# Kernel optimization log

Hardware: AMD Instinct MI355X
Metric: run time of the kernel (lower is better)

The kernel has to match this reference:

```python
import jax, jax.numpy as jnp
import numpy as np

T, B, E, H = 2048, 2, 1024, 16
HD = E // H  # 64


def _apply_rope(x, sin_pos, cos_pos):
    # x: [B*H, T, HD]; rotate-half interleaved variant
    rot = jnp.stack([-x[..., 1::2], x[..., ::2]], axis=-1).reshape(x.shape)
    return x * cos_pos + rot * sin_pos


def setup_inputs() -> dict:
    key = jax.random.key(0)
    ks = jax.random.split(key, 6)
    scale_in = (6.0 / (3 * E + E)) ** 0.5  # xavier_uniform bound
    scale_out = (6.0 / (E + E)) ** 0.5
    return {
        "query": jax.random.normal(ks[0], (T, B, E), dtype=jnp.float32),
        "rel_pos": jax.random.normal(ks[1], (1, T, HD), dtype=jnp.float32),
        "in_proj_weight": jax.random.uniform(ks[2], (3 * E, E), jnp.float32, -scale_in, scale_in),
        "in_proj_bias": jnp.zeros((3 * E,), jnp.float32),
        "out_proj_weight": jax.random.uniform(ks[3], (E, E), jnp.float32, -scale_out, scale_out),
        "out_proj_bias": jnp.zeros((E,), jnp.float32),
    }


def reference(query, rel_pos, in_proj_weight, in_proj_bias, out_proj_weight, out_proj_bias):
    tgt_len, bsz, embed_dim = query.shape
    scaling = HD ** -0.5
    # fused QKV projection: F.linear(query, W, b) with W [3E, E]
    qkv = jnp.einsum("tbe,fe->tbf", query, in_proj_weight) + in_proj_bias
    q, k, v = jnp.split(qkv, 3, axis=-1)
    q = q * scaling
    # [T, B, E] -> [B*H, T, HD]
    def split_heads(x):
        return jnp.transpose(x.reshape(tgt_len, bsz * H, HD), (1, 0, 2))
    q, k, v = split_heads(q), split_heads(k), split_heads(v)
    # rotary embedding: sin, cos = rel_pos.chunk(2, -1), duplicated interleaved
    sin, cos = rel_pos[..., : HD // 2], rel_pos[..., HD // 2 :]
    sin_pos = jnp.stack([sin, sin], axis=-1).reshape(rel_pos.shape)
    cos_pos = jnp.stack([cos, cos], axis=-1).reshape(rel_pos.shape)
    q = _apply_rope(q, sin_pos, cos_pos)
    k = _apply_rope(k, sin_pos, cos_pos)
    # attention
    attn_weights = jnp.einsum("bqd,bkd->bqk", q, k)  # [B*H, T, T]
    attn_weights = jax.nn.softmax(attn_weights, axis=-1)
    attn = jnp.einsum("bqk,bkd->bqd", attn_weights, v)
    # [B*H, T, HD] -> [T, B, E]
    attn = jnp.transpose(attn, (1, 0, 2)).reshape(tgt_len, bsz, embed_dim)
    out = jnp.einsum("tbe,fe->tbf", attn, out_proj_weight) + out_proj_bias
    return out
```

## Files before the change

kernel.cpp:

```cpp
#include <hip/hip_runtime.h>

#define T_  2048
#define B_  2
#define E_  1024
#define H_  16
#define HD_ 64
#define M_  4096
#define N_QKV 3072

typedef unsigned short u16;
typedef unsigned int   u32;
typedef __attribute__((ext_vector_type(8))) __bf16 bf16x8;
typedef __attribute__((ext_vector_type(4))) float  f32x4;

__device__ inline u16 f2bf(float f) {
  u32 u = __float_as_uint(f);
  u += 0x7fffu + ((u >> 16) & 1u);
  return (u16)(u >> 16);
}

__device__ inline u32 cvtpk(float lo, float hi) {
  u32 r;
  asm("v_cvt_pk_bf16_f32 %0, %1, %2" : "=v"(r) : "v"(lo), "v"(hi));
  return r;
}

__device__ inline void gl_lds16(const u16* g, u16* l) {
  __builtin_amdgcn_global_load_lds(
      (const __attribute__((address_space(1))) u32*)g,
      (__attribute__((address_space(3))) u32*)l, 16, 0, 0);
}

__device__ inline int xcd_swz(int orig, int nwg) {
  return (orig & 7) * (nwg >> 3) + (orig >> 3);
}

__global__ __launch_bounds__(256) void cvt_kernel(
    const float* __restrict__ q, const float* __restrict__ wi,
    const float* __restrict__ wo, u16* __restrict__ X,
    u16* __restrict__ Wi, u16* __restrict__ Wo) {
  int idx = blockIdx.x * 256 + threadIdx.x;
  const int n1 = (M_ * E_) / 4, n2 = (3 * E_ * E_) / 4;
  const float4* src; u16* dst; int i;
  if (idx < n1)            { src = (const float4*)q;  dst = X;  i = idx; }
  else if (idx < n1 + n2)  { src = (const float4*)wi; dst = Wi; i = idx - n1; }
  else                     { src = (const float4*)wo; dst = Wo; i = idx - n1 - n2; }
  float4 v = src[i];
  uint2 o;
  o.x = (u32)f2bf(v.x) | ((u32)f2bf(v.y) << 16);
  o.y = (u32)f2bf(v.z) | ((u32)f2bf(v.w) << 16);
  *(uint2*)&dst[(size_t)i * 4] = o;
}

__global__ __launch_bounds__(256) void gemm_qkv(
    const u16* __restrict__ X, const u16* __restrict__ W,
    const float* __restrict__ bias, const float* __restrict__ rel,
    u16* __restrict__ qb, u16* __restrict__ kp, u16* __restrict__ vp) {
  const int K = E_;
  __shared__ u16 SH[16384];
  u16 (*As)[4096] = (u16(*)[4096])SH;
  u16 (*Bs)[4096] = (u16(*)[4096])(SH + 8192);
  int orig = blockIdx.y * gridDim.x + blockIdx.x;
  int wgid = xcd_swz(orig, 32 * 24);
  const int tm = (wgid & 31) * 128, tn = (wgid >> 5) * 128;
  const int tid = threadIdx.x;
  const int w = tid >> 6, lane = tid & 63, lr = lane & 15, lg = lane >> 4;
  const int wm = (w >> 1) * 64, wn = (w & 1) * 64;
  auto stage = [&](int buf, int k0) {
    #pragma unroll
    for (int hh = 0; hh < 2; ++hh) {
      int ca = (w * 2 + hh) * 64 + lane;
      int ga = ca ^ ((ca >> 3) & 3);
      gl_lds16(X + (size_t)(tm + (ga >> 2)) * K + k0 + (ga & 3) * 8,
               &As[buf][(w * 2 + hh) * 512]);
      gl_lds16(W + (size_t)(tn + (ga >> 2)) * K + k0 + (ga & 3) * 8,
               &Bs[buf][(w * 2 + hh) * 512]);
    }
  };
  f32x4 acc[4][4] = {};
  stage(0, 0);
  __syncthreads();
  for (int it = 0; it < 32; ++it) {
    int cur = it & 1;
    if (it < 31) stage(cur ^ 1, (it + 1) * 32);
    bf16x8 af[4], bq[4];
    #pragma unroll
    for (int mi = 0; mi < 4; ++mi) {
      int ga = (wm + mi * 16 + lr) * 4 + lg; ga ^= (ga >> 3) & 3;
      af[mi] = *(const bf16x8*)&As[cur][ga * 8];
    }
    #pragma unroll
    for (int ni = 0; ni < 4; ++ni) {
      int ga = (wn + ni * 16 + lr) * 4 + lg; ga ^= (ga >> 3) & 3;
      bq[ni] = *(const bf16x8*)&Bs[cur][ga * 8];
    }
    #pragma unroll
    for (int mi = 0; mi < 4; ++mi)
      #pragma unroll
      for (int ni = 0; ni < 4; ++ni)
        acc[mi][ni] = __builtin_amdgcn_mfma_f32_16x16x32_bf16(
            af[mi], bq[ni], acc[mi][ni], 0, 0, 0);
    __syncthreads();
  }
  const int sect = tn >> 10;
  #pragma unroll
  for (int ni = 0; ni < 4; ++ni) {
    int n = tn + wn + ni * 16 + lr;
    float bv = bias[n];
    int nn = n & 1023;
    int d = nn & 63, i2 = d >> 1;
    int hsub = (nn >> 6) & 1;
    #pragma unroll
    for (int mi = 0; mi < 4; ++mi) {
      #pragma unroll
      for (int r = 0; r < 4; ++r) {
        int m = tm + wm + mi * 16 + lg * 4 + r;
        int t = m >> 1, bb = m & 1, tl = t & 63;
        float v = acc[mi][ni][r] + bv;
        if (sect == 0) v *= 0.125f;
        if (sect < 2) {
          float partner = __shfl_xor(v, 1);
          float sp = rel[t * HD_ + i2];
          float cp = rel[t * HD_ + 32 + i2];
          float rot = (d & 1) ? partner : -partner;
          v = v * cp + rot * sp;
        }
        int off;
        if (sect == 0)
          off = tl * 64 + d;
        else if (sect == 1)
          off = (((tl >> 4) * 2 + (d >> 5)) << 9)
              + (((d >> 3) & 3) << 7) + ((tl & 15) << 3) + (d & 7);
        else
          off = (((tl >> 5) * 4 + (d >> 4)) << 9)
              + (((tl >> 3) & 3) << 7) + ((d & 15) << 3) + (tl & 7);
        SH[((bb << 1) | hsub) * 4096 + off] = f2bf(v);
      }
    }
  }
  __syncthreads();
  {
    int h0 = (tn & 1023) >> 6;
    int bb = w >> 1, hs = w & 1;
    int bh = bb * H_ + h0 + hs;
    int t0 = tm >> 1;
    u16* dst;
    if (sect == 0)      dst = qb + ((size_t)bh * T_ + t0) * HD_;
    else if (sect == 1) dst = kp + (((size_t)bh * 32 + (t0 >> 6)) << 12);
    else                dst = vp + (((size_t)bh * 32 + (t0 >> 6)) << 12);
    const u16* srcp = SH + w * 4096;
    #pragma unroll
    for (int i = 0; i < 8; ++i)
      *(uint4*)&dst[(size_t)(i * 64 + lane) * 8] =
          *(const uint4*)&srcp[(i * 64 + lane) * 8];
  }
}

__global__ __launch_bounds__(256, 4) void attn_kernel(
    const u16* __restrict__ qbm, const u16* __restrict__ kp,
    const u16* __restrict__ vp, u16* __restrict__ attnb) {
  __shared__ u16 Kl[2][4096];
  __shared__ u16 Vl[2][4096];
  int orig = blockIdx.y * gridDim.x + blockIdx.x;
  int wgid = xcd_swz(orig, 32 * 32);
  int bh = wgid >> 5;
  int tid = threadIdx.x;
  int w = tid >> 6, lane = tid & 63, lr = lane & 15, lg = lane >> 4;
  int qbase = (wgid & 31) * 64 + w * 16;
  const u16* qrow  = qbm + (size_t)bh * T_ * HD_;
  const u16* ktile = kp + ((size_t)bh * 32) * 4096;
  const u16* vtile = vp + ((size_t)bh * 32) * 4096;
  bf16x8 qf[2];
  #pragma unroll
  for (int ks = 0; ks < 2; ++ks)
    qf[ks] = *(const bf16x8*)&qrow[(size_t)(qbase + lr) * HD_ + ks * 32 + lg * 8];
  const int cb0 = w * 128, cb1 = w * 128 + 64;
  gl_lds16(ktile + (size_t)(cb0 + lane) * 8, &Kl[0][cb0 * 8]);
  gl_lds16(ktile + (size_t)(cb1 + lane) * 8, &Kl[0][cb1 * 8]);
  gl_lds16(vtile + (size_t)(cb0 + lane) * 8, &Vl[0][cb0 * 8]);
  gl_lds16(vtile + (size_t)(cb1 + lane) * 8, &Vl[0][cb1 * 8]);
  f32x4 o[4] = {};
  float mrun = -INFINITY, lrun = 0.f;
  __syncthreads();
  for (int kt = 0; kt < 32; ++kt) {
    int cur = kt & 1;
    if (kt < 31) {
      const u16* kn = ktile + ((size_t)(kt + 1)) * 4096;
      const u16* vn = vtile + ((size_t)(kt + 1)) * 4096;
      gl_lds16(kn + (size_t)(cb0 + lane) * 8, &Kl[cur ^ 1][cb0 * 8]);
      gl_lds16(kn + (size_t)(cb1 + lane) * 8, &Kl[cur ^ 1][cb1 * 8]);
      gl_lds16(vn + (size_t)(cb0 + lane) * 8, &Vl[cur ^ 1][cb0 * 8]);
      gl_lds16(vn + (size_t)(cb1 + lane) * 8, &Vl[cur ^ 1][cb1 * 8]);
    }
    f32x4 st[4];
    #pragma unroll
    for (int kb4 = 0; kb4 < 4; ++kb4) {
      st[kb4] = (f32x4){0.f, 0.f, 0.f, 0.f};
      #pragma unroll
      for (int ks = 0; ks < 2; ++ks) {
        bf16x8 a = *(const bf16x8*)&Kl[cur][(kb4 * 2 + ks) * 512 + lane * 8];
        st[kb4] = __builtin_amdgcn_mfma_f32_16x16x32_bf16(a, qf[ks], st[kb4], 0, 0, 0);
      }
    }
    float mx = -INFINITY;
    #pragma unroll
    for (int kb4 = 0; kb4 < 4; ++kb4)
      #pragma unroll
      for (int r = 0; r < 4; ++r) mx = fmaxf(mx, st[kb4][r]);
    mx = fmaxf(mx, __shfl_xor(mx, 16));
    mx = fmaxf(mx, __shfl_xor(mx, 32));
    if (!__all(mx <= mrun + 8.f)) {
      float mnew = fmaxf(mrun, mx);
      float sc = __expf(mrun - mnew);
      lrun *= sc;
      #pragma unroll
      for (int db = 0; db < 4; ++db) o[db] *= sc;
      mrun = mnew;
    }
    float ls = 0.f;
    u32 cv[4][2];
    #pragma unroll
    for (int kb4 = 0; kb4 < 4; ++kb4) {
      float p0 = __expf(st[kb4][0] - mrun);
      float p1 = __expf(st[kb4][1] - mrun);
      float p2 = __expf(st[kb4][2] - mrun);
      float p3 = __expf(st[kb4][3] - mrun);
      ls += (p0 + p1) + (p2 + p3);
      cv[kb4][0] = cvtpk(p0, p1);
      cv[kb4][1] = cvtpk(p2, p3);
    }
    ls += __shfl_xor(ls, 16);
    ls += __shfl_xor(ls, 32);
    lrun += ls;
    #pragma unroll
    for (int ks = 0; ks < 2; ++ks) {
      u32 a = cv[ks * 2][0], b = cv[ks * 2][1];
      u32 c = cv[ks * 2 + 1][0], d = cv[ks * 2 + 1][1];
      asm("v_permlane32_swap_b32 %0, %1" : "+v"(a), "+v"(c));
      asm("v_permlane32_swap_b32 %0, %1" : "+v"(b), "+v"(d));
      asm("v_permlane16_swap_b32 %0, %1" : "+v"(a), "+v"(c));
      asm("v_permlane16_swap_b32 %0, %1" : "+v"(b), "+v"(d));
      u32 pf32[4] = {a, b, c, d};
      bf16x8 pf = *(const bf16x8*)pf32;
      #pragma unroll
      for (int db = 0; db < 4; ++db) {
        bf16x8 vf = *(const bf16x8*)&Vl[cur][(ks * 4 + db) * 512 + lane * 8];
        o[db] = __builtin_amdgcn_mfma_f32_16x16x32_bf16(vf, pf, o[db], 0, 0, 0);
      }
    }
    __syncthreads();
  }
  float inv = 1.f / lrun;
  int bb = bh >> 4, h = bh & 15;
  int m = (qbase + lr) * 2 + bb;
  #pragma unroll
  for (int db = 0; db < 4; ++db) {
    uint2 u;
    u.x = cvtpk(o[db][0] * inv, o[db][1] * inv);
    u.y = cvtpk(o[db][2] * inv, o[db][3] * inv);
    *(uint2*)&attnb[(size_t)m * E_ + h * 64 + db * 16 + lg * 4] = u;
  }
}

__global__ __launch_bounds__(256) void gemm_out(
    const u16* __restrict__ A, const u16* __restrict__ W,
    const float* __restrict__ bias, float* __restrict__ out) {
  const int K = E_;
  __shared__ u16 As[2][4096];
  __shared__ u16 Bs[2][4096];
  int orig = blockIdx.y * gridDim.x + blockIdx.x;
  int wgid = xcd_swz(orig, 32 * 8);
  const int tm = (wgid & 31) * 128, tn = (wgid >> 5) * 128;
  const int tid = threadIdx.x;
  const int w = tid >> 6, lane = tid & 63, lr = lane & 15, lg = lane >> 4;
  const int wm = (w >> 1) * 64, wn = (w & 1) * 64;
  auto stage = [&](int buf, int k0) {
    #pragma unroll
    for (int hh = 0; hh < 2; ++hh) {
      int ca = (w * 2 + hh) * 64 + lane;
      int ga = ca ^ ((ca >> 3) & 3);
      gl_lds16(A + (size_t)(tm + (ga >> 2)) * K + k0 + (ga & 3) * 8,
               &As[buf][(w * 2 + hh) * 512]);
      gl_lds16(W + (size_t)(tn + (ga >> 2)) * K + k0 + (ga & 3) * 8,
               &Bs[buf][(w * 2 + hh) * 512]);
    }
  };
  f32x4 acc[4][4] = {};
  stage(0, 0);
  __syncthreads();
  for (int it = 0; it < 32; ++it) {
    int cur = it & 1;
    if (it < 31) stage(cur ^ 1, (it + 1) * 32);
    bf16x8 af[4], bq[4];
    #pragma unroll
    for (int mi = 0; mi < 4; ++mi) {
      int ga = (wm + mi * 16 + lr) * 4 + lg; ga ^= (ga >> 3) & 3;
      af[mi] = *(const bf16x8*)&As[cur][ga * 8];
    }
    #pragma unroll
    for (int ni = 0; ni < 4; ++ni) {
      int ga = (wn + ni * 16 + lr) * 4 + lg; ga ^= (ga >> 3) & 3;
      bq[ni] = *(const bf16x8*)&Bs[cur][ga * 8];
    }
    #pragma unroll
    for (int mi = 0; mi < 4; ++mi)
      #pragma unroll
      for (int ni = 0; ni < 4; ++ni)
        acc[mi][ni] = __builtin_amdgcn_mfma_f32_16x16x32_bf16(
            af[mi], bq[ni], acc[mi][ni], 0, 0, 0);
    __syncthreads();
  }
  #pragma unroll
  for (int ni = 0; ni < 4; ++ni) {
    int n = tn + wn + ni * 16 + lr;
    float bv = bias[n];
    #pragma unroll
    for (int mi = 0; mi < 4; ++mi) {
      #pragma unroll
      for (int r = 0; r < 4; ++r) {
        int m = tm + wm + mi * 16 + lg * 4 + r;
        out[(size_t)m * E_ + n] = acc[mi][ni][r] + bv;
      }
    }
  }
}

extern "C" void kernel_launch(void* const* d_in, const int* in_sizes, int n_in,
                              void* d_out, int out_size, void* d_ws, size_t ws_size,
                              hipStream_t stream) {
  const float* q   = (const float*)d_in[0];
  const float* rel = (const float*)d_in[1];
  const float* wi  = (const float*)d_in[2];
  const float* bi  = (const float*)d_in[3];
  const float* wo  = (const float*)d_in[4];
  const float* bo  = (const float*)d_in[5];
  float* out = (float*)d_out;
  char* ws = (char*)d_ws;
  u16* Xb  = (u16*)(ws);
  u16* Wib = (u16*)(ws + 8388608);
  u16* Wob = (u16*)(ws + 14680064);
  u16* qb  = (u16*)(ws + 16777216);
  u16* kpb = (u16*)(ws + 25165824);
  u16* vpb = (u16*)(ws + 33554432);
  u16* attnb = Xb;

  cvt_kernel<<<dim3(8192), dim3(256), 0, stream>>>(q, wi, wo, Xb, Wib, Wob);
  gemm_qkv<<<dim3(32, 24), dim3(256), 0, stream>>>(Xb, Wib, bi, rel, qb, kpb, vpb);
  attn_kernel<<<dim3(32, 32), dim3(256), 0, stream>>>(qb, kpb, vpb, attnb);
  gemm_out<<<dim3(32, 8), dim3(256), 0, stream>>>(attnb, Wob, bo, out);
}
```

Before: 139.6 us.

## Use partial vmcnt waits with raw barriers and base-2 softmax exponent

Replaces __syncthreads in the GEMM and attention loops with explicit s_waitcnt vmcnt(4) plus raw s_barrier, so the next tile's global-to-LDS loads can stay in flight while the current tile is consumed. It also folds log2(e) into the Q scaling (0.125*1.4427) so softmax can use exp2f instead of __expf, and raises the rescale threshold to match the base-2 domain. The risk is correctness: with the wait placed after the prefetch issue, vmcnt(4) only guarantees the older loads landed, and the hand-written counts and compiler fences must match the actual number of outstanding loads per thread.

Result: slower. 153.4 us (+9.9%).

```diff
diff --git a/kernel.cpp b/kernel.cpp
--- a/kernel.cpp
+++ b/kernel.cpp
@@ -34,6 +34,9 @@
 __device__ inline int xcd_swz(int orig, int nwg) {
   return (orig & 7) * (nwg >> 3) + (orig >> 3);
 }
+
+#define BAR()   __builtin_amdgcn_s_barrier()
+#define FENCE() asm volatile("" ::: "memory")
 
 __global__ __launch_bounds__(256) void cvt_kernel(
     const float* __restrict__ q, const float* __restrict__ wi,
@@ -79,10 +82,16 @@
   };
   f32x4 acc[4][4] = {};
   stage(0, 0);
-  __syncthreads();
   for (int it = 0; it < 32; ++it) {
     int cur = it & 1;
-    if (it < 31) stage(cur ^ 1, (it + 1) * 32);
+    if (it < 31) {
+      stage(cur ^ 1, (it + 1) * 32);
+      asm volatile("s_waitcnt vmcnt(4)" ::: "memory");
+    } else {
+      asm volatile("s_waitcnt vmcnt(0)" ::: "memory");
+    }
+    BAR();
+    FENCE();
     bf16x8 af[4], bq[4];
     #pragma unroll
     for (int mi = 0; mi < 4; ++mi) {
@@ -100,7 +109,8 @@
       for (int ni = 0; ni < 4; ++ni)
         acc[mi][ni] = __builtin_amdgcn_mfma_f32_16x16x32_bf16(
             af[mi], bq[ni], acc[mi][ni], 0, 0, 0);
-    __syncthreads();
+    FENCE();
+    BAR();
   }
   const int sect = tn >> 10;
   #pragma unroll
@@ -117,7 +127,7 @@
         int m = tm + wm + mi * 16 + lg * 4 + r;
         int t = m >> 1, bb = m & 1, tl = t & 63;
         float v = acc[mi][ni][r] + bv;
-        if (sect == 0) v *= 0.125f;
+        if (sect == 0) v *= 0.18033688f;
         if (sect < 2) {
           float partner = __shfl_xor(v, 1);
           float sp = rel[t * HD_ + i2];
@@ -175,23 +185,27 @@
   for (int ks = 0; ks < 2; ++ks)
     qf[ks] = *(const bf16x8*)&qrow[(size_t)(qbase + lr) * HD_ + ks * 32 + lg * 8];
   const int cb0 = w * 128, cb1 = w * 128 + 64;
-  gl_lds16(ktile + (size_t)(cb0 + lane) * 8, &Kl[0][cb0 * 8]);
-  gl_lds16(ktile + (size_t)(cb1 + lane) * 8, &Kl[0][cb1 * 8]);
-  gl_lds16(vtile + (size_t)(cb0 + lane) * 8, &Vl[0][cb0 * 8]);
-  gl_lds16(vtile + (size_t)(cb1 + lane) * 8, &Vl[0][cb1 * 8]);
+  auto stage = [&](int buf, int kt) {
+    const u16* kn = ktile + ((size_t)kt) * 4096;
+    const u16* vn = vtile + ((size_t)kt) * 4096;
+    gl_lds16(kn + (size_t)(cb0 + lane) * 8, &Kl[buf][cb0 * 8]);
+    gl_lds16(kn + (size_t)(cb1 + lane) * 8, &Kl[buf][cb1 * 8]);
+    gl_lds16(vn + (size_t)(cb0 + lane) * 8, &Vl[buf][cb0 * 8]);
+    gl_lds16(vn + (size_t)(cb1 + lane) * 8, &Vl[buf][cb1 * 8]);
+  };
   f32x4 o[4] = {};
   float mrun = -INFINITY, lrun = 0.f;
-  __syncthreads();
+  stage(0, 0);
   for (int kt = 0; kt < 32; ++kt) {
     int cur = kt & 1;
     if (kt < 31) {
-      const u16* kn = ktile + ((size_t)(kt + 1)) * 4096;
-      const u16* vn = vtile + ((size_t)(kt + 1)) * 4096;
-      gl_lds16(kn + (size_t)(cb0 + lane) * 8, &Kl[cur ^ 1][cb0 * 8]);
-      gl_lds16(kn + (size_t)(cb1 + lane) * 8, &Kl[cur ^ 1][cb1 * 8]);
-      gl_lds16(vn + (size_t)(cb0 + lane) * 8, &Vl[cur ^ 1][cb0 * 8]);
-      gl_lds16(vn + (size_t)(cb1 + lane) * 8, &Vl[cur ^ 1][cb1 * 8]);
-    }
+      stage(cur ^ 1, kt + 1);
+      asm volatile("s_waitcnt vmcnt(4)" ::: "memory");
+    } else {
+      asm volatile("s_waitcnt vmcnt(0)" ::: "memory");
+    }
+    BAR();
+    FENCE();
     f32x4 st[4];
     #pragma unroll
     for (int kb4 = 0; kb4 < 4; ++kb4) {
@@ -209,9 +223,9 @@
       for (int r = 0; r < 4; ++r) mx = fmaxf(mx, st[kb4][r]);
     mx = fmaxf(mx, __shfl_xor(mx, 16));
     mx = fmaxf(mx, __shfl_xor(mx, 32));
-    if (!__all(mx <= mrun + 8.f)) {
+    if (!__all(mx <= mrun + 11.5f)) {
       float mnew = fmaxf(mrun, mx);
-      float sc = __expf(mrun - mnew);
+      float sc = exp2f(mrun - mnew);
       lrun *= sc;
       #pragma unroll
       for (int db = 0; db < 4; ++db) o[db] *= sc;
@@ -221,10 +235,10 @@
     u32 cv[4][2];
     #pragma unroll
     for (int kb4 = 0; kb4 < 4; ++kb4) {
-      float p0 = __expf(st[kb4][0] - mrun);
-      float p1 = __expf(st[kb4][1] - mrun);
-      float p2 = __expf(st[kb4][2] - mrun);
-      float p3 = __expf(st[kb4][3] - mrun);
+      float p0 = exp2f(st[kb4][0] - mrun);
+      float p1 = exp2f(st[kb4][1] - mrun);
+      float p2 = exp2f(st[kb4][2] - mrun);
+      float p3 = exp2f(st[kb4][3] - mrun);
       ls += (p0 + p1) + (p2 + p3);
       cv[kb4][0] = cvtpk(p0, p1);
       cv[kb4][1] = cvtpk(p2, p3);
@@ -248,7 +262,8 @@
         o[db] = __builtin_amdgcn_mfma_f32_16x16x32_bf16(vf, pf, o[db], 0, 0, 0);
       }
     }
-    __syncthreads();
+    FENCE();
+    BAR();
   }
   float inv = 1.f / lrun;
   int bb = bh >> 4, h = bh & 15;
@@ -287,10 +302,16 @@
   };
   f32x4 acc[4][4] = {};
   stage(0, 0);
-  __syncthreads();
   for (int it = 0; it < 32; ++it) {
     int cur = it & 1;
-    if (it < 31) stage(cur ^ 1, (it + 1) * 32);
+    if (it < 31) {
+      stage(cur ^ 1, (it + 1) * 32);
+      asm volatile("s_waitcnt vmcnt(4)" ::: "memory");
+    } else {
+      asm volatile("s_waitcnt vmcnt(0)" ::: "memory");
+    }
+    BAR();
+    FENCE();
     bf16x8 af[4], bq[4];
     #pragma unroll
     for (int mi = 0; mi < 4; ++mi) {
@@ -308,7 +329,8 @@
       for (int ni = 0; ni < 4; ++ni)
         acc[mi][ni] = __builtin_amdgcn_mfma_f32_16x16x32_bf16(
             af[mi], bq[ni], acc[mi][ni], 0, 0, 0);
-    __syncthreads();
+    FENCE();
+    BAR();
   }
   #pragma unroll
   for (int ni = 0; ni < 4; ++ni) {
```
